# Optimization experiments

Measured on AMD Instinct MI355X. Metric: run time of the kernel, lower is better.

## Reference

```python
import jax, jax.numpy as jnp
import numpy as np


def _grid_sample_bilinear_zeros(src, y, x):
    """Bilinear grid_sample, zeros padding, pixel-space coords.
    src: [B,C,H,W]; y,x: [B,H,W] float pixel coordinates (y along H, x along W).
    Returns [B,C,H,W].
    """
    B, C, H, W = src.shape
    y0 = jnp.floor(y)
    x0 = jnp.floor(x)
    y1 = y0 + 1.0
    x1 = x0 + 1.0
    wy1 = y - y0
    wy0 = 1.0 - wy1
    wx1 = x - x0
    wx0 = 1.0 - wx1

    b_idx = jnp.arange(B)[:, None, None]  # [B,1,1]

    def gather(yi, xi):
        valid = ((yi >= 0) & (yi < H) & (xi >= 0) & (xi < W)).astype(src.dtype)
        yc = jnp.clip(yi, 0, H - 1).astype(jnp.int32)
        xc = jnp.clip(xi, 0, W - 1).astype(jnp.int32)
        v = src[b_idx, :, yc, xc]  # advanced indexing -> [B,H,W,C]
        return v * valid[..., None]

    out = (gather(y0, x0) * (wy0 * wx0)[..., None]
           + gather(y0, x1) * (wy0 * wx1)[..., None]
           + gather(y1, x0) * (wy1 * wx0)[..., None]
           + gather(y1, x1) * (wy1 * wx1)[..., None])  # [B,H,W,C]
    return out.transpose(0, 3, 1, 2)


def setup_inputs() -> dict:
    key = jax.random.key(0)
    k1, k2 = jax.random.split(key)
    B, C, H, W = 8, 64, 256, 256
    src = jax.random.normal(k1, (B, C, H, W), dtype=jnp.float32)
    flow = jax.random.normal(k2, (B, 2, H, W), dtype=jnp.float32)
    return {"src": src, "flow": flow}


def reference(src, flow):
    B, C, H, W = src.shape
    # identity grid (meshgrid 'ij'): channel 0 = row index (H), channel 1 = col index (W)
    gy = jnp.arange(H, dtype=flow.dtype)[None, :, None]  # [1,H,1]
    gx = jnp.arange(W, dtype=flow.dtype)[None, None, :]  # [1,1,W]
    new_y = gy + flow[:, 0]  # [B,H,W]
    new_x = gx + flow[:, 1]
    # normalize to [-1,1] (as the module does) ...
    ny = 2.0 * (new_y / (H - 1) - 0.5)
    nx = 2.0 * (new_x / (W - 1) - 0.5)
    # ... then grid_sample with align_corners=True maps back to pixel space
    py = (ny + 1.0) * 0.5 * (H - 1)
    px = (nx + 1.0) * 0.5 * (W - 1)
    return _grid_sample_bilinear_zeros(src, py, px)
```

## Files before the change

kernel.cpp:

```cpp
#include <hip/hip_runtime.h>

#define B_ 8
#define C_ 64
#define H_ 256
#define W_ 256
#define RT 8
#define CG 8
#define WIN 24
#define PITCH 264

__global__ __launch_bounds__(256, 6) void st_warp_kernel(
    const float* __restrict__ src,
    const float* __restrict__ flow,
    float* __restrict__ out)
{
    __shared__ float tile[WIN * PITCH];

    const int HW = H_ * W_;

    int id    = blockIdx.x;
    int b     = id & 7;
    int local = id >> 3;
    int rt    = local & 31;
    int cg    = local >> 5;
    int r0    = rt * RT;
    int cbase = cg * CG;
    int w     = threadIdx.x;

    int ylo = r0 - 8;
    ylo = ylo < 0 ? 0 : (ylo > H_ - WIN ? H_ - WIN : ylo);

    int   o0[RT];
    float b00[RT], b01[RT], b10[RT], b11[RT];
    unsigned md = 0;

    const float* flow_b = flow + (size_t)b * 2 * HW;

    #pragma unroll
    for (int j = 0; j < RT; ++j) {
        int h = r0 + j;
        float fy = flow_b[h * W_ + w];
        float fx = flow_b[HW + h * W_ + w];
        float new_y = (float)h + fy;
        float new_x = (float)w + fx;
        float ny = 2.0f * (new_y / (float)(H_ - 1) - 0.5f);
        float nx = 2.0f * (new_x / (float)(W_ - 1) - 0.5f);
        float py = (ny + 1.0f) * 0.5f * (float)(H_ - 1);
        float px = (nx + 1.0f) * 0.5f * (float)(W_ - 1);

        float y0f = floorf(py), x0f = floorf(px);
        int y0 = (int)y0f, x0 = (int)x0f;
        int y1 = y0 + 1,  x1 = x0 + 1;
        float wy1 = py - y0f, wy0 = 1.0f - wy1;
        float wx1 = px - x0f, wx0 = 1.0f - wx1;

        bool vy0 = (y0 >= 0) & (y0 < H_);
        bool vy1 = (y1 >= 0) & (y1 < H_);
        bool vx0 = (x0 >= 0) & (x0 < W_);
        bool vx1 = (x1 >= 0) & (x1 < W_);

        float a00 = wy0 * wx0 * (float)(vy0 & vx0);
        float a01 = wy0 * wx1 * (float)(vy0 & vx1);
        float a10 = wy1 * wx0 * (float)(vy1 & vx0);
        float a11 = wy1 * wx1 * (float)(vy1 & vx1);

        int y0c = min(max(y0, 0), H_ - 1);
        int y1c = min(max(y1, 0), H_ - 1);
        int x0c = min(max(x0, 0), W_ - 1);
        int x1c = min(max(x1, 0), W_ - 1);
        int xl  = min(max(x0, 0), W_ - 2);

        bool s0 = (x0c == xl);
        bool s1 = (x1c == xl);
        b00[j] = (s0 ? a00 : 0.0f) + (s1 ? a01 : 0.0f);
        b01[j] = (s0 ? 0.0f : a00) + (s1 ? 0.0f : a01);
        b10[j] = (s0 ? a10 : 0.0f) + (s1 ? a11 : 0.0f);
        b11[j] = (s0 ? 0.0f : a10) + (s1 ? 0.0f : a11);

        int rl0 = min(max(y0c - ylo, 0), WIN - 1);
        int rl1 = min(max(y1c - ylo, 0), WIN - 1);
        o0[j] = rl0 * PITCH + xl;
        if (rl1 == rl0 + 1) md |= (1u << j);
    }

    int wv   = threadIdx.x >> 6;
    int lane = threadIdx.x & 63;

    const float* sc0 = src + ((size_t)(b * C_ + cbase)) * HW + (size_t)ylo * W_;
    float*       oc0 = out + ((size_t)(b * C_ + cbase)) * HW + (size_t)r0 * W_ + w;

    for (int c = 0; c < CG; ++c) {
        const float* sc = sc0 + (size_t)c * HW;

        #pragma unroll
        for (int it = 0; it < WIN / 4; ++it) {
            int r = it * 4 + wv;
            __builtin_amdgcn_global_load_lds(
                (const __attribute__((address_space(1))) void*)(sc + r * W_ + (lane << 2)),
                (__attribute__((address_space(3))) void*)(&tile[r * PITCH]),
                16, 0, 0);
        }
        __syncthreads();

        float* oc = oc0 + (size_t)c * HW;
        #pragma unroll
        for (int j = 0; j < RT; ++j) {
            int off0 = o0[j];
            float p0x = tile[off0], p0y = tile[off0 + 1];
            int off1 = off0 + (((md >> j) & 1) ? PITCH : 0);
            float p1x = tile[off1], p1y = tile[off1 + 1];
            float v = p0x * b00[j] + p0y * b01[j] + p1x * b10[j] + p1y * b11[j];
            __builtin_nontemporal_store(v, oc + j * W_);
        }
        __syncthreads();
    }
}

extern "C" void kernel_launch(void* const* d_in, const int* in_sizes, int n_in,
                              void* d_out, int out_size, void* d_ws, size_t ws_size,
                              hipStream_t stream) {
    const float* src  = (const float*)d_in[0];
    const float* flow = (const float*)d_in[1];
    float* out = (float*)d_out;
    dim3 grid(B_ * (H_ / RT) * (C_ / CG));
    dim3 block(256);
    st_warp_kernel<<<grid, block, 0, stream>>>(src, flow, out);
}
```

Baseline: 244.3 us.

## Double-buffer LDS source tiles to overlap channel loads with compute

Switches the shared tile to two buffers and prefetches the next channel's source window into LDS via global_load_lds while the current channel is interpolated. Manual vmcnt waits and raw barriers replace the full __syncthreads pairs, and the first tile load is hoisted ahead of the flow/weight setup. This doubles LDS use and lowers the occupancy hint from 6 to 3 blocks, which trades parallelism for overlap. The hand-counted vmcnt values must match the actual count of outstanding memory ops, including the nontemporal stores.

```diff
diff --git a/kernel.cpp b/kernel.cpp
--- a/kernel.cpp
+++ b/kernel.cpp
@@ -9,12 +9,13 @@
 #define WIN 24
 #define PITCH 264
 
-__global__ __launch_bounds__(256, 6) void st_warp_kernel(
+
+__global__ __launch_bounds__(256, 3) void st_warp_kernel(
     const float* __restrict__ src,
     const float* __restrict__ flow,
     float* __restrict__ out)
 {
-    __shared__ float tile[WIN * PITCH];
+    __shared__ float tile[2][WIN * PITCH];
 
     const int HW = H_ * W_;
 
@@ -29,6 +30,20 @@
 
     int ylo = r0 - 8;
     ylo = ylo < 0 ? 0 : (ylo > H_ - WIN ? H_ - WIN : ylo);
+
+    int wv   = threadIdx.x >> 6;
+    int lane = threadIdx.x & 63;
+
+    const float* sc0 = src + ((size_t)(b * C_ + cbase)) * HW + (size_t)ylo * W_;
+
+    #pragma unroll
+    for (int it = 0; it < WIN / 4; ++it) {
+        int r = it * 4 + wv;
+        __builtin_amdgcn_global_load_lds(
+            (const __attribute__((address_space(1))) void*)(sc0 + r * W_ + (lane << 2)),
+            (__attribute__((address_space(3))) void*)(&tile[0][r * PITCH]),
+            16, 0, 0);
+    }
 
     int   o0[RT];
     float b00[RT], b01[RT], b10[RT], b11[RT];
@@ -83,36 +98,45 @@
         if (rl1 == rl0 + 1) md |= (1u << j);
     }
 
-    int wv   = threadIdx.x >> 6;
-    int lane = threadIdx.x & 63;
+    float* oc0 = out + ((size_t)(b * C_ + cbase)) * HW + (size_t)r0 * W_ + w;
 
-    const float* sc0 = src + ((size_t)(b * C_ + cbase)) * HW + (size_t)ylo * W_;
-    float*       oc0 = out + ((size_t)(b * C_ + cbase)) * HW + (size_t)r0 * W_ + w;
+    #pragma unroll
+    for (int c = 0; c < CG; ++c) {
+        if (c + 1 < CG) {
+            const float* sc = sc0 + (size_t)(c + 1) * HW;
+            float* dst = &tile[(c + 1) & 1][0];
+            #pragma unroll
+            for (int it = 0; it < WIN / 4; ++it) {
+                int r = it * 4 + wv;
+                __builtin_amdgcn_global_load_lds(
+                    (const __attribute__((address_space(1))) void*)(sc + r * W_ + (lane << 2)),
+                    (__attribute__((address_space(3))) void*)(dst + r * PITCH),
+                    16, 0, 0);
+            }
+        }
 
-    for (int c = 0; c < CG; ++c) {
-        const float* sc = sc0 + (size_t)c * HW;
+        if (c == 0)           asm volatile("s_waitcnt vmcnt(6)"  ::: "memory");
+        else if (c == CG - 1) asm volatile("s_waitcnt vmcnt(8)"  ::: "memory");
+        else                  asm volatile("s_waitcnt vmcnt(14)" ::: "memory");
+        __builtin_amdgcn_s_barrier();
+        asm volatile("" ::: "memory");
 
-        #pragma unroll
-        for (int it = 0; it < WIN / 4; ++it) {
-            int r = it * 4 + wv;
-            __builtin_amdgcn_global_load_lds(
-                (const __attribute__((address_space(1))) void*)(sc + r * W_ + (lane << 2)),
-                (__attribute__((address_space(3))) void*)(&tile[r * PITCH]),
-                16, 0, 0);
-        }
-        __syncthreads();
-
+        const float* tl = &tile[c & 1][0];
         float* oc = oc0 + (size_t)c * HW;
         #pragma unroll
         for (int j = 0; j < RT; ++j) {
             int off0 = o0[j];
-            float p0x = tile[off0], p0y = tile[off0 + 1];
+            float p0x = tl[off0], p0y = tl[off0 + 1];
             int off1 = off0 + (((md >> j) & 1) ? PITCH : 0);
-            float p1x = tile[off1], p1y = tile[off1 + 1];
+            float p1x = tl[off1], p1y = tl[off1 + 1];
             float v = p0x * b00[j] + p0y * b01[j] + p1x * b10[j] + p1y * b11[j];
             __builtin_nontemporal_store(v, oc + j * W_);
         }
-        __syncthreads();
+
+        if (c + 1 < CG) {
+            asm volatile("" ::: "memory");
+            __builtin_amdgcn_s_barrier();
+        }
     }
 }
 
```

Measured after the change: 237.2 us. -2.9%, faster.
